# Performance work log

Hardware: AMD Instinct MI355X
Metric: run time of the kernel (lower is better)

Reference implementation:

```python
import jax, jax.numpy as jnp
import numpy as np

BIT = 64
NUM_TRAIN = 100000
N_CLASS = 100
BATCH = 128
MU = 1.0
NU = 0.1
ETA = 55.0
DCC_ITER = 10


def setup_inputs() -> dict:
    key = jax.random.key(0)
    k1, k2, k3, k4, k5 = jax.random.split(key, 5)
    u = jax.random.normal(k1, (BATCH, BIT), dtype=jnp.float32)
    y = (jax.random.uniform(k2, (BATCH, N_CLASS)) < 0.1).astype(jnp.float32)
    ind = jnp.arange(BATCH, dtype=jnp.int32)  # unique column indices into num_train
    U = jax.random.normal(k3, (BIT, NUM_TRAIN), dtype=jnp.float32)
    B = jnp.sign(jax.random.normal(k4, (BIT, NUM_TRAIN), dtype=jnp.float32))  # +-1 codes
    Ybuf = (jax.random.uniform(k5, (N_CLASS, NUM_TRAIN)) < 0.1).astype(jnp.float32)
    return {"u": u, "y": y, "ind": ind, "U": U, "B": B, "Ybuf": Ybuf}


def _update_b_and_w(B, U, Ybuf):
    # Faithful DCC: dcc_iter outer iterations; within each, W from a ridge
    # solve, then sequential sign coordinate-descent over the `bit` rows of B.
    lam_eye = (NU / MU) * jnp.eye(BIT, dtype=B.dtype)
    W = None
    for _ in range(DCC_ITER):
        # W = inv(B B^T + (nu/mu) I) @ B @ Y^T  -> (bit, n_class)
        W = jnp.linalg.solve(B @ B.T + lam_eye, B @ Ybuf.T)
        P = W @ Ybuf + (ETA / MU) * U  # (bit, num_train); constant within inner loop

        def body(Bc, i):
            w = W[i]                         # (n_class,)
            Ww = W @ w                       # (bit,)
            # B_prime.T @ W_prime @ w == B.T @ (W @ w) - B[i] * (w . w)
            row = jnp.sign(P[i] - (Ww @ Bc - Bc[i] * (w @ w)))
            return Bc.at[i].set(row), None

        B, _ = jax.lax.scan(body, B, jnp.arange(BIT))
    return B, W


def reference(u, y, ind, U, B, Ybuf):
    # buffer updates: U gets detached u (torch uses u.t().data), Y gets y
    U = U.at[:, ind].set(jax.lax.stop_gradient(u).T)
    Ybuf = Ybuf.at[:, ind].set(y.T)
    B, W = _update_b_and_w(B, U, Ybuf)

    inner_product = (u @ U) * 0.5                       # (batch, num_train)
    s = (y @ Ybuf > 0).astype(u.dtype)                  # (batch, num_train)
    likelihood = jnp.log1p(jnp.exp(-jnp.abs(inner_product))) \
        + jnp.maximum(inner_product, 0.0) - s * inner_product
    likelihood_loss = jnp.mean(likelihood)
    cl_loss = jnp.mean((y.T - W.T @ B[:, ind]) ** 2)    # (n_class, batch)
    reg_loss = jnp.mean(W ** 2)
    return likelihood_loss + MU * cl_loss + NU * reg_loss
```

## Files before the change

### kernel.cpp

```cpp
#include <hip/hip_runtime.h>
#include <cstdint>
#include <cstddef>


#define NT 100000
#define WPR 1568
#define NWREAL 1563
#define NGRPP 1568
#define NJB 1563
#define ETA_MU 55.0f
#define LAM 0.1f

typedef unsigned long long u64;
typedef _Float16 half8 __attribute__((ext_vector_type(8)));
typedef _Float16 half4 __attribute__((ext_vector_type(4)));
typedef _Float16 half2v __attribute__((ext_vector_type(2)));
typedef float float4v __attribute__((ext_vector_type(4)));

__device__ inline u64 transpose64(u64 x, int lane) {
  const u64 ms[6] = {0x5555555555555555ull,0x3333333333333333ull,0x0F0F0F0F0F0F0F0Full,
                     0x00FF00FF00FF00FFull,0x0000FFFF0000FFFFull,0x00000000FFFFFFFFull};
#pragma unroll
  for (int si = 0; si < 6; ++si) {
    int s = 1 << si;
    u64 m = ms[si];
    u64 y = __shfl_xor(x, s, 64);
    if ((lane & s) == 0) x = (x & m) | ((y & m) << s);
    else                 x = (x & ~m) | ((y & ~m) >> s);
  }
  return x;
}

__device__ inline int wave_reduce_i32(int v) {
#pragma unroll
  for (int off = 32; off > 0; off >>= 1) v += __shfl_down(v, off, 64);
  return v;
}
__device__ inline double wave_reduce_f64(double v) {
#pragma unroll
  for (int off = 32; off > 0; off >>= 1) v += __shfl_down(v, off, 64);
  return v;
}

__global__ __launch_bounds__(256) void build_colmasks(
    const float* __restrict__ B, const float* __restrict__ Ybuf,
    u64* __restrict__ Bmask, u64* __restrict__ Ymask,
    signed char* __restrict__ owner, int* __restrict__ cflags) {
  if (blockIdx.x == 0 && threadIdx.x < 16) cflags[threadIdx.x] = 0;
  int j = blockIdx.x * 256 + threadIdx.x;
  if (j >= NT) return;
  owner[j] = (signed char)-1;
  u64 bm = 0;
#pragma unroll
  for (int i = 0; i < 64; ++i)
    bm |= ((u64)(B[(size_t)i * NT + j] > 0.0f)) << i;
  u64 m0 = 0, m1 = 0;
#pragma unroll
  for (int c = 0; c < 64; ++c)
    m0 |= ((u64)(Ybuf[(size_t)c * NT + j] > 0.5f)) << c;
#pragma unroll
  for (int c = 64; c < 100; ++c)
    m1 |= ((u64)(Ybuf[(size_t)c * NT + j] > 0.5f)) << (c - 64);
  Bmask[j] = bm;
  Ymask[2 * j] = m0;
  Ymask[2 * j + 1] = m1;
}

__global__ void scatter_y(const float* __restrict__ y, const int* __restrict__ ind,
                          u64* __restrict__ Ymask, u64* __restrict__ ybatch,
                          signed char* __restrict__ owner, int* __restrict__ popcY) {
  int b = threadIdx.x;
  if (b >= 128) return;
  if (b < 100) popcY[b] = 0;
  u64 m0 = 0, m1 = 0;
  for (int c = 0; c < 100; ++c) {
    bool v = y[b * 100 + c] > 0.5f;
    if (c < 64) m0 |= ((u64)v) << c;
    else        m1 |= ((u64)v) << (c - 64);
  }
  ybatch[2 * b] = m0;
  ybatch[2 * b + 1] = m1;
  int col = ind[b];
  Ymask[2 * col] = m0;
  Ymask[2 * col + 1] = m1;
  owner[col] = (signed char)b;
}

__global__ __launch_bounds__(256) void build_rows(
    const u64* __restrict__ Bmask, const u64* __restrict__ Ymask,
    u64* __restrict__ Brow, u64* __restrict__ Yrow, int* __restrict__ popcY) {
  int g = blockIdx.x * 4 + (threadIdx.x >> 6);
  int lane = threadIdx.x & 63;
  if (g >= NGRPP) return;
  int j = g * 64 + lane;
  bool act = j < NT;
  u64 bm = act ? Bmask[j] : 0ull;
  u64 y0 = act ? Ymask[2 * j] : 0ull;
  u64 y1 = act ? Ymask[2 * j + 1] : 0ull;
  u64 tb = transpose64(bm, lane);
  Brow[(size_t)lane * WPR + g] = tb;
  u64 t0 = transpose64(y0, lane);
  Yrow[(size_t)lane * WPR + g] = t0;
  atomicAdd(&popcY[lane], (int)__popcll(t0));
  u64 t1 = transpose64(y1, lane);
  if (lane < 36) {
    Yrow[(size_t)(64 + lane) * WPR + g] = t1;
    atomicAdd(&popcY[64 + lane], (int)__popcll(t1));
  }
}

__global__ __launch_bounds__(256, 4) void k1_sr(
    const u64* __restrict__ Brow, const u64* __restrict__ Yrow,
    int* __restrict__ S_part, int* __restrict__ R_part,
    int it, const int* __restrict__ cflags) {
  if (it > 0 && cflags[it - 1] == 0) return;
  int k = blockIdx.x;
  int q = blockIdx.y;
  int w0 = q * 196;
  int wv = threadIdx.x >> 6, lane = threadIdx.x & 63;
  u64 tmask = (lane < 4) ? ~0ull : 0ull;
  const u64* bk = Brow + (size_t)k * WPR + w0;
  u64 b0 = bk[lane], b1 = bk[lane + 64], b2 = bk[lane + 128];
  u64 b3 = bk[192 + (lane & 3)] & tmask;
  int sS[16];
#pragma unroll
  for (int m = 0; m < 16; ++m) {
    const u64* br = Brow + (size_t)(4 * m + wv) * WPR + w0;
    u64 x0 = br[lane], x1 = br[lane + 64], x2 = br[lane + 128];
    u64 x3 = br[192 + (lane & 3)] & tmask;
    sS[m] = __popcll(x0 ^ b0) + __popcll(x1 ^ b1) +
            __popcll(x2 ^ b2) + __popcll(x3 ^ b3);
  }
  int sR[25];
#pragma unroll
  for (int m = 0; m < 25; ++m) {
    const u64* yr = Yrow + (size_t)(4 * m + wv) * WPR + w0;
    u64 x0 = yr[lane], x1 = yr[lane + 64], x2 = yr[lane + 128];
    u64 x3 = yr[192 + (lane & 3)] & tmask;
    sR[m] = __popcll(x0 & b0) + __popcll(x1 & b1) +
            __popcll(x2 & b2) + __popcll(x3 & b3);
  }
#pragma unroll
  for (int off = 32; off > 0; off >>= 1) {
#pragma unroll
    for (int m = 0; m < 16; ++m) sS[m] += __shfl_down(sS[m], off, 64);
#pragma unroll
    for (int m = 0; m < 25; ++m) sR[m] += __shfl_down(sR[m], off, 64);
  }
  if (lane == 0) {
#pragma unroll
    for (int m = 0; m < 16; ++m)
      S_part[q * 4096 + k * 64 + 4 * m + wv] = sS[m];
#pragma unroll
    for (int m = 0; m < 25; ++m)
      R_part[q * 6400 + k * 100 + 4 * m + wv] = sR[m];
  }
}

__global__ __launch_bounds__(256, 1) void k2a_solve(
    const int* __restrict__ S_part, const int* __restrict__ R_part,
    const int* __restrict__ popcY, float* __restrict__ Wr,
    float* __restrict__ Wc, int it, const int* __restrict__ cflags) {
  if (it > 0 && cflags[it - 1] == 0) return;
  __shared__ short sEi[4096];
  __shared__ _Float16 sXa[64 * 32];
  __shared__ _Float16 sXb[64 * 32];
  int tid = threadIdx.x;
  int wv = tid >> 6, k = tid & 63;
  int b = blockIdx.x;
  const int qbase_t[4] = {0, 7, 14, 20};
  const int qcnt_t[4]  = {7, 7, 6, 6};
  int qbase = qbase_t[b], Q = qcnt_t[b];
  const int off7[4] = {0, 2, 4, 6}, cnt7[4] = {2, 2, 2, 1};
  const int off6[4] = {0, 2, 4, 5}, cnt6[4] = {2, 2, 1, 1};
  int woff = (Q == 7) ? off7[wv] : off6[wv];
  int wcnt = (Q == 7) ? cnt7[wv] : cnt6[wv];
  const float alpha = 1.0f / (100000.0f + LAM);
  for (int e = tid; e < 4096; e += 256) {
    int kk = e >> 6, ll = e & 63;
    int mm = 0;
#pragma unroll
    for (int qq = 0; qq < 8; ++qq) mm += S_part[qq * 4096 + e];
    int v = (kk == ll) ? 0 : (NT - 2 * mm);
    v = v > 32767 ? 32767 : (v < -32767 ? -32767 : v);
    sEi[kk * 64 + (ll ^ (kk & 31))] = (short)v;
  }
  float4 rr4[2], xf[2];
#pragma unroll
  for (int q = 0; q < 2; ++q) {
    if (q < wcnt) {
      float tmp[4];
#pragma unroll
      for (int e4 = 0; e4 < 4; ++e4) {
        int cg = 4 * (qbase + woff + q) + e4;
        float rv = 0.0f;
        if (cg < 100) {
          int rr = 0;
#pragma unroll
          for (int qq = 0; qq < 8; ++qq) rr += R_part[qq * 6400 + k * 100 + cg];
          rv = (float)(2 * rr - popcY[cg]);
        }
        tmp[e4] = rv;
      }
      rr4[q] = make_float4(tmp[0], tmp[1], tmp[2], tmp[3]);
      xf[q] = make_float4(alpha * tmp[0], alpha * tmp[1],
                          alpha * tmp[2], alpha * tmp[3]);
    }
  }
  if (wcnt == 2) {
    half8 h;
    h[0] = (_Float16)xf[0].x; h[1] = (_Float16)xf[0].y;
    h[2] = (_Float16)xf[0].z; h[3] = (_Float16)xf[0].w;
    h[4] = (_Float16)xf[1].x; h[5] = (_Float16)xf[1].y;
    h[6] = (_Float16)xf[1].z; h[7] = (_Float16)xf[1].w;
    *(half8*)&sXa[k * 32 + 4 * woff] = h;
  } else {
    half4 h;
    h[0] = (_Float16)xf[0].x; h[1] = (_Float16)xf[0].y;
    h[2] = (_Float16)xf[0].z; h[3] = (_Float16)xf[0].w;
    *(half4*)&sXa[k * 32 + 4 * woff] = h;
  }
  __syncthreads();
  _Float16* Xs = sXa;
  _Float16* Xd = sXb;
  for (int it2 = 0; it2 < 4; ++it2) {
    float4 a4[2];
#pragma unroll
    for (int q = 0; q < 2; ++q)
      if (q < wcnt) a4[q] = rr4[q];
    if (wcnt == 2) {
      for (int l = 0; l < 64; ++l) {
        float ev = (float)sEi[k * 64 + (l ^ (k & 31))];
        half8 x8 = *(const half8*)&Xs[l * 32 + 4 * woff];
        a4[0].x -= ev * (float)x8[0]; a4[0].y -= ev * (float)x8[1];
        a4[0].z -= ev * (float)x8[2]; a4[0].w -= ev * (float)x8[3];
        a4[1].x -= ev * (float)x8[4]; a4[1].y -= ev * (float)x8[5];
        a4[1].z -= ev * (float)x8[6]; a4[1].w -= ev * (float)x8[7];
      }
    } else {
      for (int l = 0; l < 64; ++l) {
        float ev = (float)sEi[k * 64 + (l ^ (k & 31))];
        half4 x4 = *(const half4*)&Xs[l * 32 + 4 * woff];
        a4[0].x -= ev * (float)x4[0]; a4[0].y -= ev * (float)x4[1];
        a4[0].z -= ev * (float)x4[2]; a4[0].w -= ev * (float)x4[3];
      }
    }
#pragma unroll
    for (int q = 0; q < 2; ++q) {
      if (q < wcnt) {
        xf[q] = make_float4(alpha * a4[q].x, alpha * a4[q].y,
                            alpha * a4[q].z, alpha * a4[q].w);
      }
    }
    if (it2 < 3) {
      if (wcnt == 2) {
        half8 h;
        h[0] = (_Float16)xf[0].x; h[1] = (_Float16)xf[0].y;
        h[2] = (_Float16)xf[0].z; h[3] = (_Float16)xf[0].w;
        h[4] = (_Float16)xf[1].x; h[5] = (_Float16)xf[1].y;
        h[6] = (_Float16)xf[1].z; h[7] = (_Float16)xf[1].w;
        *(half8*)&Xd[k * 32 + 4 * woff] = h;
      } else {
        half4 h;
        h[0] = (_Float16)xf[0].x; h[1] = (_Float16)xf[0].y;
        h[2] = (_Float16)xf[0].z; h[3] = (_Float16)xf[0].w;
        *(half4*)&Xd[k * 32 + 4 * woff] = h;
      }
      __syncthreads();
      _Float16* t = Xs; Xs = Xd; Xd = t;
    }
  }
#pragma unroll
  for (int q = 0; q < 2; ++q) {
    if (q < wcnt) {
      float v4[4] = {xf[q].x, xf[q].y, xf[q].z, xf[q].w};
#pragma unroll
      for (int e4 = 0; e4 < 4; ++e4) {
        int cg = 4 * (qbase + woff + q) + e4;
        if (cg < 100) {
          Wr[k * 100 + cg] = v4[e4];
          Wc[cg * 64 + k] = v4[e4];
        }
      }
    }
  }
}

__global__ __launch_bounds__(256, 1) void k2b_gram(
    const float* __restrict__ Wr, float* __restrict__ G,
    int it, const int* __restrict__ cflags) {
  if (it > 0 && cflags[it - 1] == 0) return;
  __shared__ float sX[6400];
  int tid = threadIdx.x, wv = tid >> 6, k = tid & 63;
  for (int t = tid; t < 6400; t += 256) sX[t] = Wr[t];
  __syncthreads();
  float4 xl[25];
#pragma unroll
  for (int q = 0; q < 25; ++q) xl[q] = *(const float4*)&sX[k * 100 + 4 * q];
#pragma unroll
  for (int ii = 0; ii < 4; ++ii) {
    int i = blockIdx.x * 16 + wv * 4 + ii;
    const float4* xi = (const float4*)&sX[i * 100];
    float d0 = 0.f, d1 = 0.f, d2 = 0.f, d3 = 0.f;
#pragma unroll
    for (int q = 0; q < 25; ++q) {
      float4 a = xi[q];
      d0 += xl[q].x * a.x; d1 += xl[q].y * a.y;
      d2 += xl[q].z * a.z; d3 += xl[q].w * a.w;
    }
    G[i * 64 + k] = (d0 + d1) + (d2 + d3);
  }
}

__global__ __launch_bounds__(256, 2) void k3_gs(
    const float* __restrict__ U, const float* __restrict__ u,
    const signed char* __restrict__ owner, const float* __restrict__ Wc,
    const float* __restrict__ Gm, u64* __restrict__ Bmask,
    u64* __restrict__ Brow, const u64* __restrict__ Ymask,
    int it, int* __restrict__ cflags) {
  if (it > 0 && cflags[it - 1] == 0) return;
  __shared__ _Float16 sWt[64 * 136];
  __shared__ _Float16 sGr[64 * 72];
  __shared__ float sGd[64];
  __shared__ _Float16 sQx[4 * 64 * 72];
  int tid = threadIdx.x;
  for (int t = tid; t < 8192; t += 256) {
    int i = t & 63, c = t >> 6;
    sWt[i * 136 + c] = (c < 100) ? (_Float16)Wc[c * 64 + i] : (_Float16)0.0f;
  }
  for (int t = tid; t < 4096; t += 256) {
    int i = t >> 6, k = t & 63;
    sGr[i * 72 + k] = (_Float16)Gm[t];
  }
  if (tid < 64) sGd[tid] = Gm[tid * 65];
  __syncthreads();
  int wv = tid >> 6, lane = tid & 63;
  int g = blockIdx.x * 4 + wv;
  int n15 = lane & 15, quad = lane >> 4;
  int j = g * 64 + lane;
  bool act = j < NT;
  int jc = act ? j : NT - 1;
  u64 bm = Bmask[jc];
  u64 y0 = Ymask[2 * jc], y1 = Ymask[2 * jc + 1];
  half8 aW[4][4], aG[4][2];
#pragma unroll
  for (int mt = 0; mt < 4; ++mt) {
    int rb = mt * 16 + n15;
#pragma unroll
    for (int kt = 0; kt < 4; ++kt)
      aW[mt][kt] = *(const half8*)&sWt[rb * 136 + kt * 32 + quad * 8];
#pragma unroll
    for (int kt = 0; kt < 2; ++kt)
      aG[mt][kt] = *(const half8*)&sGr[rb * 72 + kt * 32 + quad * 8];
  }
  _Float16* xq = &sQx[wv * 64 * 72];
  int c0q = quad * 8;
#pragma unroll
  for (int nt = 0; nt < 4; ++nt) {
    int src = nt * 16 + n15;
    u64 cy0 = __shfl(y0, src, 64);
    u64 cy1 = __shfl(y1, src, 64);
    u64 cbm = __shfl(bm, src, 64);
    half8 yf[4], bf[2];
#pragma unroll
    for (int kt = 0; kt < 2; ++kt) {
      int c0 = kt * 32 + c0q;
      u64 w = cy0 >> c0;
      w |= (c0 ? (cy1 << ((64 - c0) & 63)) : 0ull);
#pragma unroll
      for (int e = 0; e < 8; ++e)
        yf[kt][e] = ((w >> e) & 1ull) ? (_Float16)1.0f : (_Float16)0.0f;
    }
#pragma unroll
    for (int kt = 2; kt < 4; ++kt) {
      int c0 = (kt - 2) * 32 + c0q;
      u64 w = cy1 >> c0;
#pragma unroll
      for (int e = 0; e < 8; ++e)
        yf[kt][e] = ((w >> e) & 1ull) ? (_Float16)1.0f : (_Float16)0.0f;
    }
#pragma unroll
    for (int kt = 0; kt < 2; ++kt) {
      int c0 = kt * 32 + c0q;
      u64 w = cbm >> c0;
#pragma unroll
      for (int e = 0; e < 8; ++e)
        bf[kt][e] = ((w >> e) & 1ull) ? (_Float16)-1.0f : (_Float16)1.0f;
    }
#pragma unroll
    for (int mt = 0; mt < 4; ++mt) {
      float4v c = {0.f, 0.f, 0.f, 0.f};
#pragma unroll
      for (int kt = 0; kt < 4; ++kt)
        c = __builtin_amdgcn_mfma_f32_16x16x32_f16(aW[mt][kt], yf[kt], c, 0, 0, 0);
#pragma unroll
      for (int kt = 0; kt < 2; ++kt)
        c = __builtin_amdgcn_mfma_f32_16x16x32_f16(aG[mt][kt], bf[kt], c, 0, 0, 0);
      half4 hs;
      hs[0] = (_Float16)c[0]; hs[1] = (_Float16)c[1];
      hs[2] = (_Float16)c[2]; hs[3] = (_Float16)c[3];
      *(half4*)&xq[(nt * 16 + n15) * 72 + mt * 16 + quad * 4] = hs;
    }
  }
  int ow = owner[jc];
  float p[64];
  if (ow >= 0) {
#pragma unroll
    for (int i = 0; i < 64; ++i) p[i] = ETA_MU * u[ow * 64 + i];
  } else {
#pragma unroll
    for (int i = 0; i < 64; ++i) p[i] = ETA_MU * U[(size_t)i * NT + jc];
  }
  half8 qx[8];
#pragma unroll
  for (int t = 0; t < 8; ++t)
    qx[t] = *(const half8*)&xq[lane * 72 + t * 8];
  u64 cm = bm;
#pragma unroll
  for (int i = 0; i < 64; ++i) {
    bool ob = (cm >> i) & 1ull;
    float val = p[i] + (float)qx[i >> 3][i & 7] + (ob ? sGd[i] : -sGd[i]);
    bool nb = val > 0.0f;
    bool ch = (nb != ob);
    if (__any(ch)) {
      _Float16 dl = ch ? (nb ? (_Float16)2.0f : (_Float16)-2.0f) : (_Float16)0.0f;
#pragma unroll
      for (int t = 0; t < 8; ++t) {
        half8 gr = *(const half8*)&sGr[i * 72 + t * 8];
        qx[t] -= gr * dl;
      }
      if (ch) cm ^= (1ull << i);
    }
  }
  u64 nm = act ? cm : 0ull;
  bool chg = act && (nm != bm);
  if (__any(chg) && lane == 0) cflags[it] = 1;
  if (act) Bmask[j] = nm;
  u64 tb = transpose64(nm, lane);
  Brow[(size_t)lane * WPR + g] = tb;
}

__global__ __launch_bounds__(256, 4) void l1_like(
    const float* __restrict__ U, const float* __restrict__ u,
    const signed char* __restrict__ owner, const u64* __restrict__ Ymask,
    const u64* __restrict__ ybatch, double* __restrict__ partial) {
  __shared__ _Float16 shu[8192];
  __shared__ u64 sy[256];
  __shared__ double wred[4];
  int tid = threadIdx.x;
  for (int e = tid; e < 1024; e += 256) {
    int b = e >> 3, k8 = e & 7;
    const float4* src = (const float4*)&u[b * 64 + k8 * 8];
    float4 f0 = src[0], f1 = src[1];
    half8 h;
    h[0] = (_Float16)f0.x; h[1] = (_Float16)f0.y;
    h[2] = (_Float16)f0.z; h[3] = (_Float16)f0.w;
    h[4] = (_Float16)f1.x; h[5] = (_Float16)f1.y;
    h[6] = (_Float16)f1.z; h[7] = (_Float16)f1.w;
    *(half8*)&shu[b * 64 + ((k8 ^ (b & 7)) * 8)] = h;
  }
  if (tid < 256) sy[tid] = ybatch[tid];
  __syncthreads();
  int wv = tid >> 6, lane = tid & 63;
  int n = lane & 15, q = lane >> 4;
  int j = blockIdx.x * 64 + wv * 16 + n;
  bool actj = j < NT;
  int jc = actj ? j : NT - 1;
  int ow = owner[jc];
  half8 bf0, bf1;
#pragma unroll
  for (int t = 0; t < 8; ++t) {
    int k = q * 8 + t;
    bf0[t] = (_Float16)U[(size_t)k * NT + jc];
    bf1[t] = (_Float16)U[(size_t)(k + 32) * NT + jc];
  }
  if (ow >= 0) {
#pragma unroll
    for (int t = 0; t < 8; ++t) {
      bf0[t] = (_Float16)u[ow * 64 + q * 8 + t];
      bf1[t] = (_Float16)u[ow * 64 + 32 + q * 8 + t];
    }
  }
  u64 ym0 = Ymask[2 * jc], ym1 = Ymask[2 * jc + 1];
  float lsum = 0.0f;
#pragma unroll
  for (int t8 = 0; t8 < 8; ++t8) {
    int brow = t8 * 16 + n;
    half8 a0 = *(const half8*)&shu[brow * 64 + ((q ^ (brow & 7)) * 8)];
    half8 a1 = *(const half8*)&shu[brow * 64 + (((q + 4) ^ (brow & 7)) * 8)];
    float4v c = {0.f, 0.f, 0.f, 0.f};
    c = __builtin_amdgcn_mfma_f32_16x16x32_f16(a0, bf0, c, 0, 0, 0);
    c = __builtin_amdgcn_mfma_f32_16x16x32_f16(a1, bf1, c, 0, 0, 0);
#pragma unroll
    for (int r = 0; r < 4; ++r) {
      int b = t8 * 16 + q * 4 + r;
      float ip = 0.5f * c[r];
      u64 yb0 = sy[2 * b], yb1 = sy[2 * b + 1];
      bool s = ((yb0 & ym0) | (yb1 & ym1)) != 0ull;
      float a = fabsf(ip);
      lsum += __logf(1.0f + __expf(-a)) + fmaxf(ip, 0.0f) - (s ? ip : 0.0f);
    }
  }
  if (!actj) lsum = 0.0f;
  double lsd = wave_reduce_f64((double)lsum);
  if (lane == 0) wred[wv] = lsd;
  __syncthreads();
  if (tid == 0)
    partial[blockIdx.x] = wred[0] + wred[1] + wred[2] + wred[3];
}

__global__ __launch_bounds__(256) void l2_fin(
    const float* __restrict__ Wr, const float* __restrict__ y,
    const int* __restrict__ ind, const u64* __restrict__ Bmask,
    const double* __restrict__ partial, float* __restrict__ out) {
  __shared__ float sw[6400];
  __shared__ u64 sbm[128];
  __shared__ double dred[12];
  int tid = threadIdx.x;
  for (int t = tid; t < 6400; t += 256) sw[t] = Wr[t];
  if (tid < 128) sbm[tid] = Bmask[ind[tid]];
  __syncthreads();
  double cls = 0.0, regs = 0.0, l1s = 0.0;
  for (int e = tid; e < 12800; e += 256) {
    int c = e >> 7, b = e & 127;
    u64 bm = sbm[b];
    float s = 0.0f;
#pragma unroll
    for (int i = 0; i < 64; ++i) {
      float w = sw[i * 100 + c];
      s += ((bm >> i) & 1ull) ? w : -w;
    }
    float d = y[b * 100 + c] - s;
    cls += (double)(d * d);
  }
  for (int e = tid; e < 6400; e += 256) {
    float w = sw[e];
    regs += (double)(w * w);
  }
  for (int t = tid; t < NJB; t += 256) l1s += partial[t];
  cls = wave_reduce_f64(cls);
  regs = wave_reduce_f64(regs);
  l1s = wave_reduce_f64(l1s);
  int wv = tid >> 6;
  if ((tid & 63) == 0) { dred[wv] = cls; dred[4 + wv] = regs; dred[8 + wv] = l1s; }
  __syncthreads();
  if (tid == 0) {
    double c = dred[0] + dred[1] + dred[2] + dred[3];
    double r = dred[4] + dred[5] + dred[6] + dred[7];
    double l = dred[8] + dred[9] + dred[10] + dred[11];
    out[0] = (float)(l * (1.0 / 12800000.0) + c * (1.0 / 12800.0) +
                     r * (0.1 / 6400.0));
  }
}

extern "C" void kernel_launch(void* const* d_in, const int* in_sizes, int n_in,
                              void* d_out, int out_size, void* d_ws, size_t ws_size,
                              hipStream_t stream) {
  const float* u    = (const float*)d_in[0];
  const float* y    = (const float*)d_in[1];
  const int*   ind  = (const int*)d_in[2];
  const float* U    = (const float*)d_in[3];
  const float* B    = (const float*)d_in[4];
  const float* Ybuf = (const float*)d_in[5];
  char* ws = (char*)d_ws;
  int* cflags        = (int*)ws;
  u64* Bmask         = (u64*)(ws + 256);
  u64* Ymask         = (u64*)(ws + 800256);
  u64* Brow          = (u64*)(ws + 2400256);
  u64* Yrow          = (u64*)(ws + 3203072);
  u64* ybatch        = (u64*)(ws + 4457472);
  int* popcY         = (int*)(ws + 4459520);
  int* S_part        = (int*)(ws + 4460032);
  int* R_part        = (int*)(ws + 4591104);
  float* Wr          = (float*)(ws + 4795904);
  float* Wc          = (float*)(ws + 4821504);
  float* G           = (float*)(ws + 4847104);
  signed char* owner = (signed char*)(ws + 4863488);
  double* partial    = (double*)(ws + 4963520);

  build_colmasks<<<391, 256, 0, stream>>>(B, Ybuf, Bmask, Ymask, owner, cflags);
  scatter_y<<<1, 128, 0, stream>>>(y, ind, Ymask, ybatch, owner, popcY);
  build_rows<<<392, 256, 0, stream>>>(Bmask, Ymask, Brow, Yrow, popcY);
  for (int it = 0; it < 10; ++it) {
    k1_sr<<<dim3(64, 8), 256, 0, stream>>>(Brow, Yrow, S_part, R_part, it, cflags);
    k2a_solve<<<4, 256, 0, stream>>>(S_part, R_part, popcY, Wr, Wc, it, cflags);
    k2b_gram<<<4, 256, 0, stream>>>(Wr, G, it, cflags);
    k3_gs<<<392, 256, 0, stream>>>(U, u, owner, Wc, G, Bmask, Brow, Ymask, it, cflags);
  }
  l1_like<<<NJB, 256, 0, stream>>>(U, u, owner, Ymask, ybatch, partial);
  l2_fin<<<1, 256, 0, stream>>>(Wr, y, ind, Bmask, partial, (float*)d_out);
}
```

Measured before the change: 559.7 us.

## Fuse Gram matrix into k3_gs via MFMA and parallelize final loss reduction

Drops the separate k2b_gram kernel, which ran on 4 blocks. Each k3_gs block now recomputes G = W W^T from its fp16 shared copy of W using MFMA instructions and writes the result into shared memory. This removes one launch per DCC iteration (10 in total) and the global round-trip for G, at the cost of redundant per-block compute and G being built from fp16 W rather than fp32. The single-block final loss kernel is also split into a 32-block partial reduction followed by a tiny finishing kernel.

```diff
diff --git a/kernel.cpp b/kernel.cpp
--- a/kernel.cpp
+++ b/kernel.cpp
@@ -31,11 +31,6 @@
   return x;
 }
 
-__device__ inline int wave_reduce_i32(int v) {
-#pragma unroll
-  for (int off = 32; off > 0; off >>= 1) v += __shfl_down(v, off, 64);
-  return v;
-}
 __device__ inline double wave_reduce_f64(double v) {
 #pragma unroll
   for (int off = 32; off > 0; off >>= 1) v += __shfl_down(v, off, 64);
@@ -286,38 +281,11 @@
   }
 }
 
-__global__ __launch_bounds__(256, 1) void k2b_gram(
-    const float* __restrict__ Wr, float* __restrict__ G,
-    int it, const int* __restrict__ cflags) {
-  if (it > 0 && cflags[it - 1] == 0) return;
-  __shared__ float sX[6400];
-  int tid = threadIdx.x, wv = tid >> 6, k = tid & 63;
-  for (int t = tid; t < 6400; t += 256) sX[t] = Wr[t];
-  __syncthreads();
-  float4 xl[25];
-#pragma unroll
-  for (int q = 0; q < 25; ++q) xl[q] = *(const float4*)&sX[k * 100 + 4 * q];
-#pragma unroll
-  for (int ii = 0; ii < 4; ++ii) {
-    int i = blockIdx.x * 16 + wv * 4 + ii;
-    const float4* xi = (const float4*)&sX[i * 100];
-    float d0 = 0.f, d1 = 0.f, d2 = 0.f, d3 = 0.f;
-#pragma unroll
-    for (int q = 0; q < 25; ++q) {
-      float4 a = xi[q];
-      d0 += xl[q].x * a.x; d1 += xl[q].y * a.y;
-      d2 += xl[q].z * a.z; d3 += xl[q].w * a.w;
-    }
-    G[i * 64 + k] = (d0 + d1) + (d2 + d3);
-  }
-}
-
 __global__ __launch_bounds__(256, 2) void k3_gs(
     const float* __restrict__ U, const float* __restrict__ u,
     const signed char* __restrict__ owner, const float* __restrict__ Wc,
-    const float* __restrict__ Gm, u64* __restrict__ Bmask,
-    u64* __restrict__ Brow, const u64* __restrict__ Ymask,
-    int it, int* __restrict__ cflags) {
+    u64* __restrict__ Bmask, u64* __restrict__ Brow,
+    const u64* __restrict__ Ymask, int it, int* __restrict__ cflags) {
   if (it > 0 && cflags[it - 1] == 0) return;
   __shared__ _Float16 sWt[64 * 136];
   __shared__ _Float16 sGr[64 * 72];
@@ -328,11 +296,6 @@
     int i = t & 63, c = t >> 6;
     sWt[i * 136 + c] = (c < 100) ? (_Float16)Wc[c * 64 + i] : (_Float16)0.0f;
   }
-  for (int t = tid; t < 4096; t += 256) {
-    int i = t >> 6, k = t & 63;
-    sGr[i * 72 + k] = (_Float16)Gm[t];
-  }
-  if (tid < 64) sGd[tid] = Gm[tid * 65];
   __syncthreads();
   int wv = tid >> 6, lane = tid & 63;
   int g = blockIdx.x * 4 + wv;
@@ -342,13 +305,40 @@
   int jc = act ? j : NT - 1;
   u64 bm = Bmask[jc];
   u64 y0 = Ymask[2 * jc], y1 = Ymask[2 * jc + 1];
-  half8 aW[4][4], aG[4][2];
+  half8 aW[4][4];
 #pragma unroll
   for (int mt = 0; mt < 4; ++mt) {
     int rb = mt * 16 + n15;
 #pragma unroll
     for (int kt = 0; kt < 4; ++kt)
       aW[mt][kt] = *(const half8*)&sWt[rb * 136 + kt * 32 + quad * 8];
+  }
+  half8 aWv[4];
+  {
+    int rb = wv * 16 + n15;
+#pragma unroll
+    for (int kt = 0; kt < 4; ++kt)
+      aWv[kt] = *(const half8*)&sWt[rb * 136 + kt * 32 + quad * 8];
+  }
+#pragma unroll
+  for (int nt = 0; nt < 4; ++nt) {
+    float4v c = {0.f, 0.f, 0.f, 0.f};
+#pragma unroll
+    for (int kt = 0; kt < 4; ++kt)
+      c = __builtin_amdgcn_mfma_f32_16x16x32_f16(aWv[kt], aW[nt][kt], c, 0, 0, 0);
+#pragma unroll
+    for (int r = 0; r < 4; ++r) {
+      int gi = wv * 16 + quad * 4 + r;
+      int gk = nt * 16 + n15;
+      sGr[gi * 72 + gk] = (_Float16)c[r];
+      if (gk == gi) sGd[gi] = c[r];
+    }
+  }
+  __syncthreads();
+  half8 aG[4][2];
+#pragma unroll
+  for (int mt = 0; mt < 4; ++mt) {
+    int rb = mt * 16 + n15;
 #pragma unroll
     for (int kt = 0; kt < 2; ++kt)
       aG[mt][kt] = *(const half8*)&sGr[rb * 72 + kt * 32 + quad * 8];
@@ -509,19 +499,20 @@
     partial[blockIdx.x] = wred[0] + wred[1] + wred[2] + wred[3];
 }
 
-__global__ __launch_bounds__(256) void l2_fin(
+__global__ __launch_bounds__(256) void l2_part(
     const float* __restrict__ Wr, const float* __restrict__ y,
     const int* __restrict__ ind, const u64* __restrict__ Bmask,
-    const double* __restrict__ partial, float* __restrict__ out) {
+    const double* __restrict__ partial, double* __restrict__ part3) {
   __shared__ float sw[6400];
   __shared__ u64 sbm[128];
   __shared__ double dred[12];
-  int tid = threadIdx.x;
+  int tid = threadIdx.x, bid = blockIdx.x;
   for (int t = tid; t < 6400; t += 256) sw[t] = Wr[t];
   if (tid < 128) sbm[tid] = Bmask[ind[tid]];
   __syncthreads();
   double cls = 0.0, regs = 0.0, l1s = 0.0;
-  for (int e = tid; e < 12800; e += 256) {
+  int e0 = bid * 400;
+  for (int e = e0 + tid; e < e0 + 400; e += 256) {
     int c = e >> 7, b = e & 127;
     u64 bm = sbm[b];
     float s = 0.0f;
@@ -533,11 +524,13 @@
     float d = y[b * 100 + c] - s;
     cls += (double)(d * d);
   }
-  for (int e = tid; e < 6400; e += 256) {
+  int r0 = bid * 200;
+  for (int e = r0 + tid; e < r0 + 200; e += 256) {
     float w = sw[e];
     regs += (double)(w * w);
   }
-  for (int t = tid; t < NJB; t += 256) l1s += partial[t];
+  int t = bid * 256 + tid;
+  if (t < NJB) l1s = partial[t];
   cls = wave_reduce_f64(cls);
   regs = wave_reduce_f64(regs);
   l1s = wave_reduce_f64(l1s);
@@ -545,12 +538,27 @@
   if ((tid & 63) == 0) { dred[wv] = cls; dred[4 + wv] = regs; dred[8 + wv] = l1s; }
   __syncthreads();
   if (tid == 0) {
-    double c = dred[0] + dred[1] + dred[2] + dred[3];
-    double r = dred[4] + dred[5] + dred[6] + dred[7];
-    double l = dred[8] + dred[9] + dred[10] + dred[11];
+    part3[bid * 4 + 0] = dred[0] + dred[1] + dred[2] + dred[3];
+    part3[bid * 4 + 1] = dred[4] + dred[5] + dred[6] + dred[7];
+    part3[bid * 4 + 2] = dred[8] + dred[9] + dred[10] + dred[11];
+  }
+}
+
+__global__ void l2_fin2(const double* __restrict__ part3,
+                        float* __restrict__ out) {
+  int tid = threadIdx.x;
+  double c = 0.0, r = 0.0, l = 0.0;
+  if (tid < 32) {
+    c = part3[tid * 4 + 0];
+    r = part3[tid * 4 + 1];
+    l = part3[tid * 4 + 2];
+  }
+  c = wave_reduce_f64(c);
+  r = wave_reduce_f64(r);
+  l = wave_reduce_f64(l);
+  if (tid == 0)
     out[0] = (float)(l * (1.0 / 12800000.0) + c * (1.0 / 12800.0) +
                      r * (0.1 / 6400.0));
-  }
 }
 
 extern "C" void kernel_launch(void* const* d_in, const int* in_sizes, int n_in,
@@ -574,7 +582,7 @@
   int* R_part        = (int*)(ws + 4591104);
   float* Wr          = (float*)(ws + 4795904);
   float* Wc          = (float*)(ws + 4821504);
-  float* G           = (float*)(ws + 4847104);
+  double* part3      = (double*)(ws + 4847104);
   signed char* owner = (signed char*)(ws + 4863488);
   double* partial    = (double*)(ws + 4963520);
 
@@ -584,9 +592,9 @@
   for (int it = 0; it < 10; ++it) {
     k1_sr<<<dim3(64, 8), 256, 0, stream>>>(Brow, Yrow, S_part, R_part, it, cflags);
     k2a_solve<<<4, 256, 0, stream>>>(S_part, R_part, popcY, Wr, Wc, it, cflags);
-    k2b_gram<<<4, 256, 0, stream>>>(Wr, G, it, cflags);
-    k3_gs<<<392, 256, 0, stream>>>(U, u, owner, Wc, G, Bmask, Brow, Ymask, it, cflags);
+    k3_gs<<<392, 256, 0, stream>>>(U, u, owner, Wc, Bmask, Brow, Ymask, it, cflags);
   }
   l1_like<<<NJB, 256, 0, stream>>>(U, u, owner, Ymask, ybatch, partial);
-  l2_fin<<<1, 256, 0, stream>>>(Wr, y, ind, Bmask, partial, (float*)d_out);
-}
+  l2_part<<<32, 256, 0, stream>>>(Wr, y, ind, Bmask, partial, part3);
+  l2_fin2<<<1, 64, 0, stream>>>(part3, (float*)d_out);
+}
```

Measured after the change: 504.3 us. -9.9%, faster.
